# Performance work log

Hardware: AMD Instinct MI355X
Metric: run time of the kernel (lower is better)

Reference implementation:

```python
import jax, jax.numpy as jnp
import numpy as np

K = 7          # neighborhood kernel size (7x7)
NH = 8         # num heads


def _nbr_idx(n):
    # NATTEN-style clamped windows: window start = clip(i - K//2, 0, n-K)
    pos = jnp.arange(n)
    start = jnp.clip(pos - K // 2, 0, n - K)          # (n,)
    idx = start[:, None] + jnp.arange(K)[None, :]     # (n, K) absolute key positions
    rel = idx - pos[:, None] + (K - 1)                # (n, K) in [0, 2K-2] for rpb lookup
    return idx, rel


def _forward(x, w_qkv, b_qkv, rpb, w_proj, b_proj, w_fc1, b_fc1, w_fc2, b_fc2):
    B, C, H, W = x.shape
    hd = C // NH
    scale = hd ** -0.5

    # ---- neighborhood attention (norm0 = Identity) ----
    xp = jnp.transpose(x, (0, 2, 3, 1))                           # (B,H,W,C)
    qkv = xp @ w_qkv + b_qkv                                      # (B,H,W,3C)
    qkv = qkv.reshape(B, H, W, 3, NH, hd)
    q = qkv[:, :, :, 0] * scale                                   # (B,H,W,nh,hd)
    k = qkv[:, :, :, 1]
    v = qkv[:, :, :, 2]

    idx_h, rel_h = _nbr_idx(H)                                    # (H,K)
    idx_w, rel_w = _nbr_idx(W)                                    # (W,K)

    # gather 7x7 neighborhoods: (B,H,K,W,K,nh,hd)
    k_nbr = k[:, idx_h][:, :, :, idx_w]
    v_nbr = v[:, idx_h][:, :, :, idx_w]

    # attention logits: (B,H,W,nh,K,K)
    attn = jnp.einsum('bxynd,bxiyjnd->bxynij', q, k_nbr)
    # relative positional bias: rpb (nh, 2K-1, 2K-1) -> (nh,H,K,W,K)
    bias = rpb[:, rel_h][:, :, :, rel_w]                          # (nh,H,K,W,K)
    attn = attn + jnp.transpose(bias, (1, 3, 0, 2, 4))[None]      # (B,H,W,nh,K,K)

    attn = jax.nn.softmax(attn.reshape(B, H, W, NH, K * K), axis=-1)
    attn = attn.reshape(B, H, W, NH, K, K)

    out = jnp.einsum('bxynij,bxiyjnd->bxynd', attn, v_nbr)        # (B,H,W,nh,hd)
    out = out.reshape(B, H, W, C) @ w_proj + b_proj               # (B,H,W,C)
    x1 = jnp.transpose(out, (0, 3, 1, 2)) + x                     # residual skip0

    # ---- MLP (1x1-conv style, channels-first; norm1 = Identity) ----
    h = jnp.einsum('bchw,cf->bfhw', x1, w_fc1) + b_fc1[None, :, None, None]
    h = jax.nn.gelu(h, approximate=False)                         # torch nn.GELU (erf)
    y = jnp.einsum('bfhw,fc->bchw', h, w_fc2) + b_fc2[None, :, None, None]
    return y + x1                                                 # residual skip1


def setup_inputs() -> dict:
    key = jax.random.key(0)
    B, C, H, W = 1, 256, 64, 128
    hid = int(C * 2.0)
    ks = jax.random.split(key, 8)
    s = 0.02
    return {
        'x': jax.random.normal(ks[0], (B, C, H, W), jnp.float32),
        'w_qkv': jax.random.normal(ks[1], (C, 3 * C), jnp.float32) * s,
        'b_qkv': jnp.zeros((3 * C,), jnp.float32),
        'rpb': jax.random.normal(ks[2], (NH, 2 * K - 1, 2 * K - 1), jnp.float32) * s,
        'w_proj': jax.random.normal(ks[3], (C, C), jnp.float32) * s,
        'b_proj': jnp.zeros((C,), jnp.float32),
        'w_fc1': jax.random.normal(ks[4], (C, hid), jnp.float32) * s,
        'b_fc1': jnp.zeros((hid,), jnp.float32),
        'w_fc2': jax.random.normal(ks[5], (hid, C), jnp.float32) * s,
        'b_fc2': jnp.zeros((C,), jnp.float32),
    }


def reference(x, w_qkv, b_qkv, rpb, w_proj, b_proj, w_fc1, b_fc1, w_fc2, b_fc2):
    return _forward(x, w_qkv, b_qkv, rpb, w_proj, b_proj, w_fc1, b_fc1, w_fc2, b_fc2)
```

## Files before the change

kernel.cpp:

```cpp
#include <hip/hip_runtime.h>

typedef unsigned short ushort;
typedef short bf16x8 __attribute__((ext_vector_type(8)));
typedef float f32x4 __attribute__((ext_vector_type(4)));

static __device__ __forceinline__ ushort f2b(float f) {
  unsigned u = __builtin_bit_cast(unsigned, f);
  u = (u + 0x7fffu + ((u >> 16) & 1u)) >> 16;
  return (ushort)u;
}
static __device__ __forceinline__ float b2f(ushort b) {
  return __builtin_bit_cast(float, (unsigned)b << 16);
}

__global__ __launch_bounds__(256) void prep_kernel(
    const float* __restrict__ x,
    const float* __restrict__ w_qkv, const float* __restrict__ w_proj,
    const float* __restrict__ w_fc1, const float* __restrict__ w_fc2,
    ushort* __restrict__ xb, ushort* __restrict__ wqkvT,
    ushort* __restrict__ wprojT, ushort* __restrict__ wfc1T,
    ushort* __restrict__ wfc2T)
{
  __shared__ float tile[32][33];
  int t = blockIdx.x;
  const float* src; ushort* dst; int R, Nc, r0, c0;
  if (t < 2048)              { src = x;      dst = xb;     R = 256; Nc = 8192; r0 = (t >> 8) * 32; c0 = (t & 255) * 32; }
  else if ((t -= 2048) < 192){ src = w_qkv;  dst = wqkvT;  R = 256; Nc = 768;  r0 = (t / 24) * 32; c0 = (t % 24) * 32; }
  else if ((t -= 192) < 64)  { src = w_proj; dst = wprojT; R = 256; Nc = 256;  r0 = (t / 8) * 32;  c0 = (t % 8) * 32; }
  else if ((t -= 64) < 128)  { src = w_fc1;  dst = wfc1T;  R = 256; Nc = 512;  r0 = (t / 16) * 32; c0 = (t % 16) * 32; }
  else           { t -= 128;   src = w_fc2;  dst = wfc2T;  R = 512; Nc = 256;  r0 = (t / 8) * 32;  c0 = (t % 8) * 32; }

  const int tx = threadIdx.x & 31, ty = threadIdx.x >> 5;
  #pragma unroll
  for (int i = 0; i < 4; i++)
    tile[ty + i * 8][tx] = src[(size_t)(r0 + ty + i * 8) * Nc + c0 + tx];
  __syncthreads();
  #pragma unroll
  for (int i = 0; i < 4; i++)
    dst[(size_t)(c0 + ty + i * 8) * R + r0 + tx] = f2b(tile[tx][ty + i * 8]);
}

template<int EPI, int KD>
__global__ __launch_bounds__(256) void gemm_mfma(
    const ushort* __restrict__ A, const ushort* __restrict__ Bt,
    const float* __restrict__ bias, const float* __restrict__ R,
    const ushort* __restrict__ RS,
    void* __restrict__ C0, void* __restrict__ C1,
    int M, int N)
{
  constexpr int LDW = 136;
  __shared__ __attribute__((aligned(16))) ushort As[64 * LDW];
  __shared__ __attribute__((aligned(16))) ushort Bs[64 * LDW];

  const int bm = blockIdx.y * 64;
  const int bn = blockIdx.x * 64;
  const int t  = threadIdx.x;
  const int w    = t >> 6;
  const int lane = t & 63;
  const int wm = (w & 1) * 32;
  const int wn = (w >> 1) * 32;
  const int lm = lane & 15;
  const int kq = lane >> 4;

  f32x4 acc[2][2] = {};

  #pragma unroll
  for (int k0 = 0; k0 < KD; k0 += 128) {
    uint4 ra[4], rb[4];
    #pragma unroll
    for (int s = 0; s < 4; s++) {
      const int L = t + 256 * s;
      const int r = L >> 4, c = L & 15;
      ra[s] = *(const uint4*)(A  + (size_t)(bm + r) * KD + k0 + c * 8);
      rb[s] = *(const uint4*)(Bt + (size_t)(bn + r) * KD + k0 + c * 8);
    }
    #pragma unroll
    for (int s = 0; s < 4; s++) {
      const int L = t + 256 * s;
      const int r = L >> 4, c = L & 15;
      *(uint4*)(&As[r * LDW + c * 8]) = ra[s];
      *(uint4*)(&Bs[r * LDW + c * 8]) = rb[s];
    }
    __syncthreads();

    #pragma unroll
    for (int ks = 0; ks < 4; ks++) {
      const int ko = ks * 32 + kq * 8;
      bf16x8 a0 = *(const bf16x8*)(&As[(wm + lm)      * LDW + ko]);
      bf16x8 a1 = *(const bf16x8*)(&As[(wm + 16 + lm) * LDW + ko]);
      bf16x8 b0 = *(const bf16x8*)(&Bs[(wn + lm)      * LDW + ko]);
      bf16x8 b1 = *(const bf16x8*)(&Bs[(wn + 16 + lm) * LDW + ko]);
      acc[0][0] = __builtin_amdgcn_mfma_f32_16x16x32_bf16(a0, b0, acc[0][0], 0, 0, 0);
      acc[0][1] = __builtin_amdgcn_mfma_f32_16x16x32_bf16(a0, b1, acc[0][1], 0, 0, 0);
      acc[1][0] = __builtin_amdgcn_mfma_f32_16x16x32_bf16(a1, b0, acc[1][0], 0, 0, 0);
      acc[1][1] = __builtin_amdgcn_mfma_f32_16x16x32_bf16(a1, b1, acc[1][1], 0, 0, 0);
    }
    __syncthreads();
  }

  #pragma unroll
  for (int ti = 0; ti < 2; ti++) {
    #pragma unroll
    for (int tj = 0; tj < 2; tj++) {
      const int n  = bn + wn + tj * 16 + lm;
      const int m0 = bm + wm + ti * 16 + kq * 4;
      if (EPI == 3) {
        float4 v;
        float* vp = &v.x;
        #pragma unroll
        for (int r = 0; r < 4; r++)
          vp[r] = acc[ti][tj][r] + bias[n] + b2f(RS[(size_t)(m0 + r) * 256 + n]);
        *(float4*)((float*)C0 + (size_t)n * M + m0) = v;
      } else if (EPI == 0) {
        if (n < 512) {
          #pragma unroll
          for (int r = 0; r < 4; r++)
            ((ushort*)C0)[(size_t)(m0 + r) * N + n] = f2b(acc[ti][tj][r] + bias[n]);
        } else {
          ushort4 st;
          st.x = f2b(acc[ti][tj][0] + bias[n]);
          st.y = f2b(acc[ti][tj][1] + bias[n]);
          st.z = f2b(acc[ti][tj][2] + bias[n]);
          st.w = f2b(acc[ti][tj][3] + bias[n]);
          *(ushort4*)((ushort*)C1 + (size_t)(n - 512) * 8192 + m0) = st;
        }
      } else {
        #pragma unroll
        for (int r = 0; r < 4; r++) {
          const int m = m0 + r;
          float v = acc[ti][tj][r] + bias[n];
          if (EPI == 1) {
            v += R[(size_t)n * M + m];
            ((ushort*)C0)[(size_t)m * 256 + n] = f2b(v);
          } else {
            v = 0.5f * v * (1.0f + erff(v * 0.70710678118f));
            ((ushort*)C0)[(size_t)m * N + n] = f2b(v);
          }
        }
      }
    }
  }
}

__global__ __launch_bounds__(256, 4) void natt_mfma(
    const ushort* __restrict__ qkv, const ushort* __restrict__ vT,
    const float* __restrict__ rpb, ushort* __restrict__ att)
{
  __shared__ __attribute__((aligned(16))) ushort Plds[4][7][16][40];
  __shared__ float Rlds[4][176];

  const int w    = threadIdx.x >> 6;
  const int lane = threadIdx.x & 63;
  const int l  = lane & 15;
  const int q  = lane >> 4;
  const int tile = blockIdx.x;
  const int n    = blockIdx.y * 4 + w;
  const int ph  = tile >> 3;
  const int pw0 = (tile & 7) << 4;
  const int p0  = ph * 128 + pw0;

  int sh = ph - 3;  sh = sh < 0 ? 0 : (sh > 57 ? 57 : sh);
  int sb = pw0 - 3; sb = sb < 0 ? 0 : sb;
  const int sba = sb & ~7;

  const float L2E = 1.44269504f;
  for (int idx = lane; idx < 169; idx += 64)
    Rlds[w][idx] = rpb[n * 169 + idx] * L2E;

  bf16x8 qf = *(const bf16x8*)(qkv + (size_t)(p0 + l) * 768 + n * 32 + q * 8);

  const float KSC = 0.17677669529663689f * 1.44269504f;
  const int relh0 = sh - ph + 6;
  float rsum[4] = {0.f, 0.f, 0.f, 0.f};

  #pragma unroll
  for (int h = 0; h < 2; h++) {
    f32x4 s[7] = {};
    #pragma unroll
    for (int i = 0; i < 7; i++) {
      const int rowp = (sh + i) * 128;
      int jc = sba + h * 16 + l;
      jc = jc > 127 ? 127 : jc;
      bf16x8 kf = *(const bf16x8*)(qkv + (size_t)(rowp + jc) * 768 + 256 + n * 32 + q * 8);
      s[i] = __builtin_amdgcn_mfma_f32_16x16x32_bf16(qf, kf, s[i], 0, 0, 0);
    }
    #pragma unroll
    for (int r = 0; r < 4; r++) {
      const int pw = pw0 + q * 4 + r;
      int sw = pw - 3; sw = sw < 0 ? 0 : (sw > 121 ? 121 : sw);
      const int jc = sba + h * 16 + l;
      const bool valid = (unsigned)(jc - sw) <= 6u;
      int relw = jc - pw + 6;
      relw = relw < 0 ? 0 : (relw > 12 ? 12 : relw);
      #pragma unroll
      for (int i = 0; i < 7; i++) {
        float b = Rlds[w][(relh0 + i) * 13 + relw];
        float v = s[i][r] * KSC + b;
        v = valid ? v : -1e30f;
        float e = exp2f(v);
        rsum[r] += e;
        Plds[w][i][q * 4 + r][h * 16 + l] = f2b(e);
      }
    }
  }

  #pragma unroll
  for (int r = 0; r < 4; r++) {
    rsum[r] += __shfl_xor(rsum[r], 1);
    rsum[r] += __shfl_xor(rsum[r], 2);
    rsum[r] += __shfl_xor(rsum[r], 4);
    rsum[r] += __shfl_xor(rsum[r], 8);
  }

  f32x4 o[2] = {};
  #pragma unroll
  for (int i = 0; i < 7; i++) {
    bf16x8 pf = *(const bf16x8*)(&Plds[w][i][l][q * 8]);
    const int rowp = (sh + i) * 128;
    #pragma unroll
    for (int dh = 0; dh < 2; dh++) {
      bf16x8 vf = *(const bf16x8*)(vT + (size_t)(n * 32 + dh * 16 + l) * 8192
                                      + rowp + sba + q * 8);
      o[dh] = __builtin_amdgcn_mfma_f32_16x16x32_bf16(pf, vf, o[dh], 0, 0, 0);
    }
  }

  #pragma unroll
  for (int r = 0; r < 4; r++) {
    const float inv = 1.0f / rsum[r];
    #pragma unroll
    for (int dh = 0; dh < 2; dh++)
      att[(size_t)(p0 + q * 4 + r) * 256 + n * 32 + dh * 16 + l] = f2b(o[dh][r] * inv);
  }
}

extern "C" void kernel_launch(void* const* d_in, const int* in_sizes, int n_in,
                              void* d_out, int out_size, void* d_ws, size_t ws_size,
                              hipStream_t stream)
{
  const float* x      = (const float*)d_in[0];
  const float* w_qkv  = (const float*)d_in[1];
  const float* b_qkv  = (const float*)d_in[2];
  const float* rpb    = (const float*)d_in[3];
  const float* w_proj = (const float*)d_in[4];
  const float* b_proj = (const float*)d_in[5];
  const float* w_fc1  = (const float*)d_in[6];
  const float* b_fc1  = (const float*)d_in[7];
  const float* w_fc2  = (const float*)d_in[8];
  const float* b_fc2  = (const float*)d_in[9];
  float* out = (float*)d_out;

  const int M = 8192;
  char* ws = (char*)d_ws;
  ushort* xb     = (ushort*)(ws);
  ushort* qkv    = (ushort*)(ws + 4194304);
  ushort* x1b    = (ushort*)(ws + 16777216);
  ushort* wqkvT  = (ushort*)(ws + 20971520);
  ushort* wprojT = (ushort*)(ws + 21364736);
  ushort* wfc1T  = (ushort*)(ws + 21495808);
  ushort* wfc2T  = (ushort*)(ws + 21757952);
  ushort* vT     = (ushort*)(ws + 22020096);
  ushort* att = xb;
  ushort* h   = qkv;

  dim3 blk(256);

  prep_kernel<<<dim3(2560), blk, 0, stream>>>(
      x, w_qkv, w_proj, w_fc1, w_fc2, xb, wqkvT, wprojT, wfc1T, wfc2T);

  gemm_mfma<0, 256><<<dim3(768 / 64, M / 64), blk, 0, stream>>>(
      xb, wqkvT, b_qkv, nullptr, nullptr, qkv, vT, M, 768);

  natt_mfma<<<dim3(512, 2), blk, 0, stream>>>(qkv, vT, rpb, att);

  gemm_mfma<1, 256><<<dim3(256 / 64, M / 64), blk, 0, stream>>>(
      att, wprojT, b_proj, x, nullptr, x1b, nullptr, M, 256);

  gemm_mfma<2, 256><<<dim3(512 / 64, M / 64), blk, 0, stream>>>(
      x1b, wfc1T, b_fc1, nullptr, nullptr, h, nullptr, M, 512);

  gemm_mfma<3, 512><<<dim3(256 / 64, M / 64), blk, 0, stream>>>(
      h, wfc2T, b_fc2, nullptr, x1b, out, nullptr, M, 256);
}
```

Measured before the change: 132.9 us.

## Fuse output projection and residual into neighborhood attention kernel

The attention kernel now runs all 8 heads of a 16-pixel tile in one 512-thread block. It stages the per-head outputs in LDS, then does the 256x256 output projection with MFMA, adding the bias and the residual x directly. This removes the separate projection GEMM launch and the global round trip of the attention output. In exchange the attention grid drops to 512 blocks of 512 threads, and each block reads the whole projection weight from global or L2.

```diff
diff --git a/kernel.cpp b/kernel.cpp
--- a/kernel.cpp
+++ b/kernel.cpp
@@ -43,8 +43,7 @@
 template<int EPI, int KD>
 __global__ __launch_bounds__(256) void gemm_mfma(
     const ushort* __restrict__ A, const ushort* __restrict__ Bt,
-    const float* __restrict__ bias, const float* __restrict__ R,
-    const ushort* __restrict__ RS,
+    const float* __restrict__ bias, const ushort* __restrict__ RS,
     void* __restrict__ C0, void* __restrict__ C1,
     int M, int N)
 {
@@ -129,32 +128,30 @@
         for (int r = 0; r < 4; r++) {
           const int m = m0 + r;
           float v = acc[ti][tj][r] + bias[n];
-          if (EPI == 1) {
-            v += R[(size_t)n * M + m];
-            ((ushort*)C0)[(size_t)m * 256 + n] = f2b(v);
-          } else {
-            v = 0.5f * v * (1.0f + erff(v * 0.70710678118f));
-            ((ushort*)C0)[(size_t)m * N + n] = f2b(v);
-          }
+          v = 0.5f * v * (1.0f + erff(v * 0.70710678118f));
+          ((ushort*)C0)[(size_t)m * N + n] = f2b(v);
         }
       }
     }
   }
 }
 
-__global__ __launch_bounds__(256, 4) void natt_mfma(
+__global__ __launch_bounds__(512, 4) void natt_proj(
     const ushort* __restrict__ qkv, const ushort* __restrict__ vT,
-    const float* __restrict__ rpb, ushort* __restrict__ att)
+    const float* __restrict__ rpb, const ushort* __restrict__ wprojT,
+    const float* __restrict__ b_proj, const float* __restrict__ x,
+    ushort* __restrict__ x1b)
 {
-  __shared__ __attribute__((aligned(16))) ushort Plds[4][7][16][40];
-  __shared__ float Rlds[4][176];
+  __shared__ __attribute__((aligned(16))) ushort Plds[8][7][16][40];
+  __shared__ float Rlds[8][176];
+  ushort* att_lds = &Plds[0][0][0][0];
 
   const int w    = threadIdx.x >> 6;
   const int lane = threadIdx.x & 63;
   const int l  = lane & 15;
   const int q  = lane >> 4;
+  const int n  = w;
   const int tile = blockIdx.x;
-  const int n    = blockIdx.y * 4 + w;
   const int ph  = tile >> 3;
   const int pw0 = (tile & 7) << 4;
   const int p0  = ph * 128 + pw0;
@@ -225,12 +222,37 @@
     }
   }
 
+  __syncthreads();
+
   #pragma unroll
   for (int r = 0; r < 4; r++) {
     const float inv = 1.0f / rsum[r];
     #pragma unroll
     for (int dh = 0; dh < 2; dh++)
-      att[(size_t)(p0 + q * 4 + r) * 256 + n * 32 + dh * 16 + l] = f2b(o[dh][r] * inv);
+      att_lds[(q * 4 + r) * 264 + w * 32 + dh * 16 + l] = f2b(o[dh][r] * inv);
+  }
+  __syncthreads();
+
+  f32x4 pacc[2] = {};
+  #pragma unroll
+  for (int ks = 0; ks < 8; ks++) {
+    bf16x8 a = *(const bf16x8*)(att_lds + l * 264 + ks * 32 + q * 8);
+    #pragma unroll
+    for (int tj = 0; tj < 2; tj++) {
+      bf16x8 b = *(const bf16x8*)(wprojT + (size_t)(w * 32 + tj * 16 + l) * 256
+                                         + ks * 32 + q * 8);
+      pacc[tj] = __builtin_amdgcn_mfma_f32_16x16x32_bf16(a, b, pacc[tj], 0, 0, 0);
+    }
+  }
+  #pragma unroll
+  for (int tj = 0; tj < 2; tj++) {
+    const int n2 = w * 32 + tj * 16 + l;
+    #pragma unroll
+    for (int r = 0; r < 4; r++) {
+      const int m = p0 + q * 4 + r;
+      float v = pacc[tj][r] + b_proj[n2] + x[(size_t)n2 * 8192 + m];
+      x1b[(size_t)m * 256 + n2] = f2b(v);
+    }
   }
 }
 
@@ -260,7 +282,6 @@
   ushort* wfc1T  = (ushort*)(ws + 21495808);
   ushort* wfc2T  = (ushort*)(ws + 21757952);
   ushort* vT     = (ushort*)(ws + 22020096);
-  ushort* att = xb;
   ushort* h   = qkv;
 
   dim3 blk(256);
@@ -269,16 +290,14 @@
       x, w_qkv, w_proj, w_fc1, w_fc2, xb, wqkvT, wprojT, wfc1T, wfc2T);
 
   gemm_mfma<0, 256><<<dim3(768 / 64, M / 64), blk, 0, stream>>>(
-      xb, wqkvT, b_qkv, nullptr, nullptr, qkv, vT, M, 768);
-
-  natt_mfma<<<dim3(512, 2), blk, 0, stream>>>(qkv, vT, rpb, att);
-
-  gemm_mfma<1, 256><<<dim3(256 / 64, M / 64), blk, 0, stream>>>(
-      att, wprojT, b_proj, x, nullptr, x1b, nullptr, M, 256);
+      xb, wqkvT, b_qkv, nullptr, qkv, vT, M, 768);
+
+  natt_proj<<<dim3(512), dim3(512), 0, stream>>>(
+      qkv, vT, rpb, wprojT, b_proj, x, x1b);
 
   gemm_mfma<2, 256><<<dim3(512 / 64, M / 64), blk, 0, stream>>>(
-      x1b, wfc1T, b_fc1, nullptr, nullptr, h, nullptr, M, 512);
+      x1b, wfc1T, b_fc1, nullptr, h, nullptr, M, 512);
 
   gemm_mfma<3, 512><<<dim3(256 / 64, M / 64), blk, 0, stream>>>(
-      h, wfc2T, b_fc2, nullptr, x1b, out, nullptr, M, 256);
-}
+      h, wfc2T, b_fc2, x1b, out, nullptr, M, 256);
+}
```

After: 134.3 us. Within noise of the previous version (+1.1%).
